# Optimization experiments

Measured on AMD Instinct MI355X. Metric: run time of the kernel, lower is better.

The kernel has to match this reference:

```python
import jax, jax.numpy as jnp
import numpy as np

N_NODES = 100000
N_EDGES = 1600000
IN_CH = 512
HID_CH = 256
OUT_CH = 32
K = 10


def setup_inputs() -> dict:
    key = jax.random.key(0)
    k_x, k_e, k_w1, k_b1, k_w2, k_b2 = jax.random.split(key, 6)
    x = jax.random.normal(k_x, (N_NODES, IN_CH), dtype=jnp.float32)
    edge_index = jax.random.randint(k_e, (2, N_EDGES), 0, N_NODES, dtype=jnp.int64)
    s1 = 1.0 / np.sqrt(IN_CH)
    s2 = 1.0 / np.sqrt(HID_CH)
    W1 = jax.random.uniform(k_w1, (IN_CH, HID_CH), jnp.float32, -s1, s1)
    b1 = jax.random.uniform(k_b1, (HID_CH,), jnp.float32, -s1, s1)
    W2 = jax.random.uniform(k_w2, (HID_CH, OUT_CH), jnp.float32, -s2, s2)
    b2 = jax.random.uniform(k_b2, (OUT_CH,), jnp.float32, -s2, s2)
    gamma = jnp.ones((K + 1,), jnp.float32) / (K + 1)
    return {"x": x, "edge_index": edge_index, "W1": W1, "b1": b1,
            "W2": W2, "b2": b2, "gamma": gamma}


def reference(x, edge_index, W1, b1, W2, b2, gamma):
    # MLP (dropout is identity in eval mode)
    h = jax.nn.relu(x @ W1 + b1) @ W2 + b2  # [N, out]
    row, col = edge_index[0], edge_index[1]
    # symmetric normalization: deg over destination nodes (col)
    deg = jax.ops.segment_sum(jnp.ones((N_EDGES,), h.dtype), col,
                              num_segments=N_NODES)
    deg_inv_sqrt = jnp.where(deg > 0, jax.lax.rsqrt(jnp.maximum(deg, 1.0)), 0.0)
    norm = (deg_inv_sqrt[row] * deg_inv_sqrt[col])[:, None]  # [E, 1]
    out = gamma[0] * h
    h_k = h
    for k in range(1, K + 1):
        # one hop: gather source feats, scale, scatter-add to destinations
        h_k = jax.ops.segment_sum(norm * h_k[row], col, num_segments=N_NODES)
        out = out + gamma[k] * h_k
    return out
```

## Files before the change

### kernel.cpp

```cpp
#include <hip/hip_runtime.h>
#include <hip/hip_bf16.h>

#define NN    100000
#define NE    1600000
#define INCH  512
#define HIDCH 256
#define OUTCH 32
#define KHOPS 10
#define NEPAD (NE + 3 * NN)

typedef __attribute__((ext_vector_type(8))) short short8;
typedef __attribute__((ext_vector_type(4))) float f32x4;

#define GLOAD_LDS16(gsrc, ldst) \
  __builtin_amdgcn_global_load_lds((const __attribute__((address_space(1))) void*)(gsrc), \
                                   (__attribute__((address_space(3))) void*)(ldst), 16, 0, 0)

constexpr size_t ws_align(size_t x) { return (x + 255) & ~(size_t)255; }
constexpr size_t USZ = ws_align((size_t)(NN + 1) * 16 * 2);
constexpr size_t OSZ = ws_align((size_t)NN * 16 * 4);
constexpr size_t OFF_H1   = 0;
constexpr size_t OFF_U00  = OFF_H1   + ws_align((size_t)NN*HIDCH*2);
constexpr size_t OFF_U01  = OFF_U00  + USZ;
constexpr size_t OFF_U10  = OFF_U01  + USZ;
constexpr size_t OFF_U11  = OFF_U10  + USZ;
constexpr size_t OFF_OA0  = OFF_U11  + USZ;
constexpr size_t OFF_OA1  = OFF_OA0  + OSZ;
constexpr size_t OFF_W1TH = OFF_OA1  + OSZ;
constexpr size_t OFF_W1TL = OFF_W1TH + ws_align((size_t)HIDCH*INCH*2);
constexpr size_t OFF_W2TH = OFF_W1TL + ws_align((size_t)HIDCH*INCH*2);
constexpr size_t OFF_W2TL = OFF_W2TH + ws_align((size_t)OUTCH*HIDCH*2);
constexpr size_t OFF_DEG  = OFF_W2TL + ws_align((size_t)OUTCH*HIDCH*2);
constexpr size_t OFF_DIS  = OFF_DEG  + ws_align((size_t)NN*4);
constexpr size_t OFF_RP   = OFF_DIS  + ws_align((size_t)NN*4);
constexpr size_t OFF_CUR  = OFF_RP   + ws_align((size_t)(NN+1)*4);
constexpr size_t OFF_CSR  = OFF_CUR  + ws_align((size_t)NN*4);
constexpr size_t OFF_PART = OFF_CSR  + ws_align((size_t)NEPAD*4);
constexpr size_t OFF_OFFS = OFF_PART + ws_align(512);

__device__ __forceinline__ unsigned short bf16_rne(float f) {
  unsigned int u = __float_as_uint(f);
  u += 0x7fffu + ((u >> 16) & 1u);
  return (unsigned short)(u >> 16);
}
__device__ __forceinline__ float bf16_to_f32(unsigned short h) {
  return __uint_as_float(((unsigned int)h) << 16);
}
__device__ __forceinline__ float bflo(unsigned int w) {
  return __uint_as_float(w << 16);
}
__device__ __forceinline__ float bfhi(unsigned int w) {
  return __uint_as_float(w & 0xffff0000u);
}

__global__ __launch_bounds__(256) void k_count_deg(const int* __restrict__ col,
                                                   int* __restrict__ deg) {
  int e = blockIdx.x * 256 + threadIdx.x;
  if (e < NE) atomicAdd(&deg[col[e]], 1);
}

__global__ __launch_bounds__(256) void k_dis(const int* __restrict__ deg,
                                             float* __restrict__ dis,
                                             unsigned short* u00, unsigned short* u01,
                                             unsigned short* u10, unsigned short* u11) {
  int v = blockIdx.x * 256 + threadIdx.x;
  if (v < NN) {
    int d = deg[v];
    dis[v] = d > 0 ? rsqrtf((float)d) : 0.0f;
  }
  if (blockIdx.x == 0) {
    int t = threadIdx.x;
    if (t < 8)       ((unsigned int*)u00)[(size_t)NN * 8 + t] = 0;
    else if (t < 16) ((unsigned int*)u01)[(size_t)NN * 8 + (t - 8)] = 0;
    else if (t < 24) ((unsigned int*)u10)[(size_t)NN * 8 + (t - 16)] = 0;
    else if (t < 32) ((unsigned int*)u11)[(size_t)NN * 8 + (t - 24)] = 0;
  }
}

__global__ __launch_bounds__(256) void k_scan1(const int* __restrict__ deg,
                                               int* __restrict__ rp,
                                               int* __restrict__ part) {
  __shared__ int s[256];
  int b = blockIdx.x, t = threadIdx.x;
  int base = b * 1024 + t * 4;
  int v0 = (base + 0 < NN) ? ((deg[base + 0] + 3) & ~3) : 0;
  int v1 = (base + 1 < NN) ? ((deg[base + 1] + 3) & ~3) : 0;
  int v2 = (base + 2 < NN) ? ((deg[base + 2] + 3) & ~3) : 0;
  int v3 = (base + 3 < NN) ? ((deg[base + 3] + 3) & ~3) : 0;
  int tot = v0 + v1 + v2 + v3;
  s[t] = tot;
  __syncthreads();
  for (int d = 1; d < 256; d <<= 1) {
    int x = (t >= d) ? s[t - d] : 0;
    __syncthreads();
    s[t] += x;
    __syncthreads();
  }
  int excl = s[t] - tot;
  if (t == 255) part[b] = s[255];
  if (base + 0 < NN) rp[base + 0] = excl;
  if (base + 1 < NN) rp[base + 1] = excl + v0;
  if (base + 2 < NN) rp[base + 2] = excl + v0 + v1;
  if (base + 3 < NN) rp[base + 3] = excl + v0 + v1 + v2;
}

__global__ __launch_bounds__(128) void k_scan2(const int* __restrict__ part,
                                               int* __restrict__ offs) {
  __shared__ int s[128];
  int t = threadIdx.x;
  int v = (t < 98) ? part[t] : 0;
  s[t] = v;
  __syncthreads();
  for (int d = 1; d < 128; d <<= 1) {
    int x = (t >= d) ? s[t - d] : 0;
    __syncthreads();
    s[t] += x;
    __syncthreads();
  }
  if (t < 98) offs[t] = s[t] - v;
}

__global__ __launch_bounds__(256) void k_scan3(int* __restrict__ rp,
                                               const int* __restrict__ offs,
                                               const int* __restrict__ part,
                                               int* __restrict__ cur) {
  int b = blockIdx.x, t = threadIdx.x;
  int o = offs[b];
  int base = b * 1024 + t * 4;
#pragma unroll
  for (int j = 0; j < 4; ++j) {
    int i = base + j;
    if (i < NN) {
      int r = rp[i] + o;
      rp[i] = r;
      cur[i] = r;
    }
  }
  if (b == 0 && t == 0) rp[NN] = offs[97] + part[97];
}

__global__ __launch_bounds__(256) void k_fill(const int* __restrict__ ei,
                                              int* __restrict__ cur,
                                              int* __restrict__ csrc) {
  int e = blockIdx.x * 256 + threadIdx.x;
  if (e < NE) {
    int c = ei[NE + e];
    int p = atomicAdd(&cur[c], 1);
    csrc[p] = ei[e];
  }
}

__global__ __launch_bounds__(256) void k_pad(const int* __restrict__ cur,
                                             const int* __restrict__ rp,
                                             int* __restrict__ csrc) {
  int v = blockIdx.x * 256 + threadIdx.x;
  if (v < NN) {
    int p = cur[v], e = rp[v + 1];
    for (; p < e; ++p) csrc[p] = NN;
  }
}

__global__ __launch_bounds__(256) void k_splitT(const float* __restrict__ src,
                                                unsigned short* __restrict__ dh,
                                                unsigned short* __restrict__ dl,
                                                int K, int N) {
  int idx = blockIdx.x * 256 + threadIdx.x;
  if (idx >= K * N) return;
  int n = idx / K, k = idx - n * K;
  float v = src[(size_t)k * N + n];
  unsigned short h = bf16_rne(v);
  dh[idx] = h;
  dl[idx] = bf16_rne(v - bf16_to_f32(h));
}

__global__ __launch_bounds__(512, 2) void k_gemm1(const float* __restrict__ X,
                                                  const unsigned short* __restrict__ W1Th,
                                                  const unsigned short* __restrict__ W1Tl,
                                                  const float* __restrict__ bias1,
                                                  unsigned short* __restrict__ H1bf) {
  __shared__ __align__(16) unsigned short Ah[2][4096];
  __shared__ __align__(16) unsigned short Bh[2][8192], Bl[2][8192];
  const int t = threadIdx.x;
  const int m0 = blockIdx.x * 128;
  const int w = t >> 6, lane = t & 63;
  const int wm = w >> 2, wn = w & 3;

  const int arow = t >> 2;
  const int achk = t & 3;
  int axrow = m0 + arow; if (axrow >= NN) axrow = NN - 1;
  const float* aptr = X + (size_t)axrow * INCH + achk * 8;
  int aidx = (arow >> 4) * 512 + ((arow & 15) + achk * 16) * 8;
  aidx ^= ((aidx >> 7) & 3) << 4;
  const int aroff = (lane * 8) ^ (((lane >> 4) & 3) << 4);

  const int bn0 = (w * 16) + (lane & 15);
  const int bko = (lane >> 4) * 8;
  const unsigned short* bs0 = W1Th + (size_t)bn0 * INCH + bko;
  const unsigned short* bs1 = W1Th + (size_t)(bn0 + 128) * INCH + bko;
  const unsigned short* bs2 = W1Tl + (size_t)bn0 * INCH + bko;
  const unsigned short* bs3 = W1Tl + (size_t)(bn0 + 128) * INCH + bko;

  f32x4 acc[4][4] = {};
  float4 av0, av1;

  av0 = *(const float4*)(aptr);
  av1 = *(const float4*)(aptr + 4);
  GLOAD_LDS16(bs0, &Bh[0][w * 512]);
  GLOAD_LDS16(bs1, &Bh[0][(w + 8) * 512]);
  GLOAD_LDS16(bs2, &Bl[0][w * 512]);
  GLOAD_LDS16(bs3, &Bl[0][(w + 8) * 512]);
  {
    float af[8] = {av0.x, av0.y, av0.z, av0.w, av1.x, av1.y, av1.z, av1.w};
    short8 ah;
#pragma unroll
    for (int i = 0; i < 8; ++i) {
      unsigned int u = __float_as_uint(af[i]);
      ah[i] = (short)((u + 0x7fffu + ((u >> 16) & 1u)) >> 16);
    }
    *(short8*)&Ah[0][aidx] = ah;
  }
  __syncthreads();

#pragma unroll
  for (int it = 0; it < 16; ++it) {
    const int cur = it & 1, nxt = cur ^ 1;
    const int k0 = it * 32;
    if (it < 15) {
      av0 = *(const float4*)(aptr + k0 + 32);
      av1 = *(const float4*)(aptr + k0 + 36);
      GLOAD_LDS16(bs0 + k0 + 32, &Bh[nxt][w * 512]);
      GLOAD_LDS16(bs1 + k0 + 32, &Bh[nxt][(w + 8) * 512]);
      GLOAD_LDS16(bs2 + k0 + 32, &Bl[nxt][w * 512]);
      GLOAD_LDS16(bs3 + k0 + 32, &Bl[nxt][(w + 8) * 512]);
    }
    short8 afrag[4];
#pragma unroll
    for (int mf = 0; mf < 4; ++mf)
      afrag[mf] = *(const short8*)&Ah[cur][(wm * 4 + mf) * 512 + aroff];
#pragma unroll
    for (int nf = 0; nf < 4; ++nf) {
      short8 bfh = *(const short8*)&Bh[cur][(wn * 4 + nf) * 512 + lane * 8];
      short8 bfl = *(const short8*)&Bl[cur][(wn * 4 + nf) * 512 + lane * 8];
#pragma unroll
      for (int mf = 0; mf < 4; ++mf) {
        acc[mf][nf] = __builtin_amdgcn_mfma_f32_16x16x32_bf16(afrag[mf], bfh, acc[mf][nf], 0, 0, 0);
        acc[mf][nf] = __builtin_amdgcn_mfma_f32_16x16x32_bf16(afrag[mf], bfl, acc[mf][nf], 0, 0, 0);
      }
    }
    if (it < 15) {
      float af[8] = {av0.x, av0.y, av0.z, av0.w, av1.x, av1.y, av1.z, av1.w};
      short8 ah;
#pragma unroll
      for (int i = 0; i < 8; ++i) {
        unsigned int u = __float_as_uint(af[i]);
        ah[i] = (short)((u + 0x7fffu + ((u >> 16) & 1u)) >> 16);
      }
      *(short8*)&Ah[nxt][aidx] = ah;
    }
    __syncthreads();
  }

  const int colbase = wn * 64 + (lane & 15);
  const int rowbase = m0 + wm * 64 + ((lane >> 4) << 2);
#pragma unroll
  for (int nf = 0; nf < 4; ++nf) {
    int col = colbase + nf * 16;
    float b = bias1[col];
#pragma unroll
    for (int mf = 0; mf < 4; ++mf) {
#pragma unroll
      for (int r = 0; r < 4; ++r) {
        int row = rowbase + mf * 16 + r;
        if (row < NN) {
          float h = fmaxf(acc[mf][nf][r] + b, 0.f);
          H1bf[(size_t)row * HIDCH + col] = bf16_rne(h);
        }
      }
    }
  }
}

__global__ __launch_bounds__(256) void k_gemm2(const unsigned short* __restrict__ H1bf,
                                               const unsigned short* __restrict__ W2Th,
                                               const unsigned short* __restrict__ W2Tl,
                                               const float* __restrict__ bias2,
                                               const float* __restrict__ gamma,
                                               const float* __restrict__ dis,
                                               unsigned short* __restrict__ u00,
                                               unsigned short* __restrict__ u01,
                                               float* __restrict__ oa0,
                                               float* __restrict__ oa1) {
  __shared__ __align__(16) unsigned short A2[8192];
  __shared__ __align__(16) unsigned short B2h[2048], B2l[2048];
  const int t = threadIdx.x;
  const int m0 = blockIdx.x * 128;

  const int arow = t >> 1;
  int axrow = m0 + arow; if (axrow >= NN) axrow = NN - 1;
  const int akb = (t & 1) * 32;
  const unsigned short* ap = H1bf + (size_t)axrow * HIDCH + akb;
  const int abase = ((arow >> 4) * 2 + (akb >> 5)) * 512 + (arow & 15) * 8;

  const int bnr = t >> 3, bkq = (t & 7) * 8;
  const int bslot = ((bnr >> 4) * 2 + (bkq >> 5)) * 512 +
                    ((bnr & 15) + (((bkq & 31) >> 3) << 4)) * 8;
  const unsigned short* bhp = W2Th + (size_t)bnr * HIDCH + bkq;
  const unsigned short* blp = W2Tl + (size_t)bnr * HIDCH + bkq;

  const int w = t >> 6, lane = t & 63;

  f32x4 acc[2][2] = {};

  for (int k0 = 0; k0 < HIDCH; k0 += 64) {
    uint4 a0 = *(const uint4*)(ap + k0);
    uint4 a1 = *(const uint4*)(ap + k0 + 8);
    uint4 a2 = *(const uint4*)(ap + k0 + 16);
    uint4 a3 = *(const uint4*)(ap + k0 + 24);
    uint4 bh = *(const uint4*)(bhp + k0);
    uint4 bl = *(const uint4*)(blp + k0);

    __syncthreads();

    *(uint4*)&A2[abase + 0 * 128] = a0;
    *(uint4*)&A2[abase + 1 * 128] = a1;
    *(uint4*)&A2[abase + 2 * 128] = a2;
    *(uint4*)&A2[abase + 3 * 128] = a3;
    *(uint4*)&B2h[bslot] = bh;
    *(uint4*)&B2l[bslot] = bl;

    __syncthreads();

    const short8* AV  = (const short8*)A2;
    const short8* BHV = (const short8*)B2h;
    const short8* BLV = (const short8*)B2l;
#pragma unroll
    for (int k32 = 0; k32 < 2; ++k32) {
      short8 bfh[2], bfl[2];
#pragma unroll
      for (int nf = 0; nf < 2; ++nf) {
        bfh[nf] = BHV[(nf * 2 + k32) * 64 + lane];
        bfl[nf] = BLV[(nf * 2 + k32) * 64 + lane];
      }
#pragma unroll
      for (int mf = 0; mf < 2; ++mf) {
        short8 a = AV[((w * 2 + mf) * 2 + k32) * 64 + lane];
#pragma unroll
        for (int nf = 0; nf < 2; ++nf) {
          acc[mf][nf] = __builtin_amdgcn_mfma_f32_16x16x32_bf16(a, bfh[nf], acc[mf][nf], 0, 0, 0);
          acc[mf][nf] = __builtin_amdgcn_mfma_f32_16x16x32_bf16(a, bfl[nf], acc[mf][nf], 0, 0, 0);
        }
      }
    }
  }

  const float g0 = gamma[0];
  const int colb = lane & 15;
  const int rowb = m0 + w * 32 + ((lane >> 4) << 2);
  const float b2c0 = bias2[colb], b2c1 = bias2[16 + colb];
#pragma unroll
  for (int mf = 0; mf < 2; ++mf) {
#pragma unroll
    for (int r = 0; r < 4; ++r) {
      int row = rowb + mf * 16 + r;
      if (row < NN) {
        float dv = dis[row];
        float h0 = acc[mf][0][r] + b2c0;
        float h1 = acc[mf][1][r] + b2c1;
        size_t o = (size_t)row * 16 + colb;
        u00[o] = bf16_rne(dv * h0);
        u01[o] = bf16_rne(dv * h1);
        oa0[o] = g0 * h0;
        oa1[o] = g0 * h1;
      }
    }
  }
}

__global__ __launch_bounds__(256) void k_hop(
    const unsigned short* __restrict__ uin0, const unsigned short* __restrict__ uin1,
    unsigned short* __restrict__ uout0, unsigned short* __restrict__ uout1,
    float* __restrict__ oa0, float* __restrict__ oa1,
    const int* __restrict__ rp, const int* __restrict__ csrc,
    const float* __restrict__ dis, const float* __restrict__ gamma, int k) {
  const int bid = blockIdx.x;
  const int xcd = bid & 7;
  const int half = xcd >> 2;
  const int hidx = (bid >> 3) * 4 + (xcd & 3);
  if (hidx >= NN / 32) return;
  const unsigned short* __restrict__ Uin = half ? uin1 : uin0;
  unsigned short* __restrict__ Uout = half ? uout1 : uout0;
  float* __restrict__ oacc = half ? oa1 : oa0;

  const int t = threadIdx.x;
  const int g = t >> 3;
  const int li = t & 7;
  const int v = hidx * 32 + g;
  const int s = rp[v], e = rp[v + 1];

  float ax0 = 0.f, ay0 = 0.f, ax1 = 0.f, ay1 = 0.f;
  float ax2 = 0.f, ay2 = 0.f, ax3 = 0.f, ay3 = 0.f;
  int j = s;
  for (; j + 8 <= e; j += 8) {
    int4 sa = *(const int4*)&csrc[j];
    int4 sb = *(const int4*)&csrc[j + 4];
    unsigned int w0 = *(const unsigned int*)&Uin[(size_t)sa.x * 16 + li * 2];
    unsigned int w1 = *(const unsigned int*)&Uin[(size_t)sa.y * 16 + li * 2];
    unsigned int w2 = *(const unsigned int*)&Uin[(size_t)sa.z * 16 + li * 2];
    unsigned int w3 = *(const unsigned int*)&Uin[(size_t)sa.w * 16 + li * 2];
    unsigned int w4 = *(const unsigned int*)&Uin[(size_t)sb.x * 16 + li * 2];
    unsigned int w5 = *(const unsigned int*)&Uin[(size_t)sb.y * 16 + li * 2];
    unsigned int w6 = *(const unsigned int*)&Uin[(size_t)sb.z * 16 + li * 2];
    unsigned int w7 = *(const unsigned int*)&Uin[(size_t)sb.w * 16 + li * 2];
    ax0 += bflo(w0); ay0 += bfhi(w0);
    ax1 += bflo(w1); ay1 += bfhi(w1);
    ax2 += bflo(w2); ay2 += bfhi(w2);
    ax3 += bflo(w3); ay3 += bfhi(w3);
    ax0 += bflo(w4); ay0 += bfhi(w4);
    ax1 += bflo(w5); ay1 += bfhi(w5);
    ax2 += bflo(w6); ay2 += bfhi(w6);
    ax3 += bflo(w7); ay3 += bfhi(w7);
  }
  if (j < e) {
    int4 sa = *(const int4*)&csrc[j];
    unsigned int w0 = *(const unsigned int*)&Uin[(size_t)sa.x * 16 + li * 2];
    unsigned int w1 = *(const unsigned int*)&Uin[(size_t)sa.y * 16 + li * 2];
    unsigned int w2 = *(const unsigned int*)&Uin[(size_t)sa.z * 16 + li * 2];
    unsigned int w3 = *(const unsigned int*)&Uin[(size_t)sa.w * 16 + li * 2];
    ax0 += bflo(w0); ay0 += bfhi(w0);
    ax1 += bflo(w1); ay1 += bfhi(w1);
    ax2 += bflo(w2); ay2 += bfhi(w2);
    ax3 += bflo(w3); ay3 += bfhi(w3);
  }
  const float Sx = (ax0 + ax1) + (ax2 + ax3);
  const float Sy = (ay0 + ay1) + (ay2 + ay3);
  const float dv = dis[v];
  const float gd = gamma[k] * dv;
  const float d2 = dv * dv;
  unsigned int packed = (unsigned int)bf16_rne(d2 * Sx) |
                        ((unsigned int)bf16_rne(d2 * Sy) << 16);
  ((unsigned int*)Uout)[(size_t)v * 8 + li] = packed;
  float2 po = *(const float2*)&oacc[(size_t)v * 16 + li * 2];
  po.x = fmaf(gd, Sx, po.x);
  po.y = fmaf(gd, Sy, po.y);
  *(float2*)&oacc[(size_t)v * 16 + li * 2] = po;
}

__global__ __launch_bounds__(256) void k_merge(const float* __restrict__ oa0,
                                               const float* __restrict__ oa1,
                                               float* __restrict__ out) {
  int i4 = blockIdx.x * 256 + threadIdx.x;
  if (i4 >= NN * 8) return;
  int v = i4 >> 3;
  int j = (i4 & 7) * 4;
  const float* src = (j < 16) ? oa0 : oa1;
  float4 val = *(const float4*)&src[(size_t)v * 16 + (j & 15)];
  *(float4*)&out[(size_t)v * 32 + j] = val;
}

extern "C" void kernel_launch(void* const* d_in, const int* in_sizes, int n_in,
                              void* d_out, int out_size, void* d_ws, size_t ws_size,
                              hipStream_t stream) {
  const float* x     = (const float*)d_in[0];
  const int*   ei    = (const int*)d_in[1];
  const float* W1    = (const float*)d_in[2];
  const float* b1    = (const float*)d_in[3];
  const float* W2    = (const float*)d_in[4];
  const float* b2    = (const float*)d_in[5];
  const float* gamma = (const float*)d_in[6];
  float* out = (float*)d_out;

  char* ws = (char*)d_ws;
  unsigned short* h1bf = (unsigned short*)(ws + OFF_H1);
  unsigned short* U[2][2] = {
    {(unsigned short*)(ws + OFF_U00), (unsigned short*)(ws + OFF_U01)},
    {(unsigned short*)(ws + OFF_U10), (unsigned short*)(ws + OFF_U11)}};
  float* oa0 = (float*)(ws + OFF_OA0);
  float* oa1 = (float*)(ws + OFF_OA1);
  unsigned short* w1th = (unsigned short*)(ws + OFF_W1TH);
  unsigned short* w1tl = (unsigned short*)(ws + OFF_W1TL);
  unsigned short* w2th = (unsigned short*)(ws + OFF_W2TH);
  unsigned short* w2tl = (unsigned short*)(ws + OFF_W2TL);
  int*   deg  = (int*)(ws + OFF_DEG);
  float* dis  = (float*)(ws + OFF_DIS);
  int*   rp   = (int*)(ws + OFF_RP);
  int*   cur  = (int*)(ws + OFF_CUR);
  int*   csrc = (int*)(ws + OFF_CSR);
  int*   part = (int*)(ws + OFF_PART);
  int*   offs = (int*)(ws + OFF_OFFS);

  hipMemsetAsync(deg, 0, NN * sizeof(int), stream);

  k_splitT<<<(INCH * HIDCH + 255) / 256, 256, 0, stream>>>(W1, w1th, w1tl, INCH, HIDCH);
  k_splitT<<<(HIDCH * OUTCH + 255) / 256, 256, 0, stream>>>(W2, w2th, w2tl, HIDCH, OUTCH);

  k_count_deg<<<(NE + 255) / 256, 256, 0, stream>>>(ei + NE, deg);
  k_dis<<<(NN + 255) / 256, 256, 0, stream>>>(deg, dis, U[0][0], U[0][1], U[1][0], U[1][1]);
  k_scan1<<<98, 256, 0, stream>>>(deg, rp, part);
  k_scan2<<<1, 128, 0, stream>>>(part, offs);
  k_scan3<<<98, 256, 0, stream>>>(rp, offs, part, cur);
  k_fill<<<(NE + 255) / 256, 256, 0, stream>>>(ei, cur, csrc);
  k_pad<<<(NN + 255) / 256, 256, 0, stream>>>(cur, rp, csrc);

  k_gemm1<<<(NN + 127) / 128, 512, 0, stream>>>(x, w1th, w1tl, b1, h1bf);
  k_gemm2<<<(NN + 127) / 128, 256, 0, stream>>>(h1bf, w2th, w2tl, b2, gamma, dis,
                                                U[0][0], U[0][1], oa0, oa1);

  const int hop_grid = ((NN / 32 + 3) / 4) * 8;
  for (int k = 1; k <= KHOPS; ++k) {
    const int pin = (k - 1) & 1, pout = k & 1;
    k_hop<<<hop_grid, 256, 0, stream>>>(U[pin][0], U[pin][1], U[pout][0], U[pout][1],
                                        oa0, oa1, rp, csrc, dis, gamma, k);
  }

  k_merge<<<(NN * 8 + 255) / 256, 256, 0, stream>>>(oa0, oa1, out);
}
```

Before: 606.9 us.

## Merge split feature halves into one 32-wide layout and retile GEMM1

The propagation state is no longer split into two 16-channel halves routed to separate XCD groups. It now uses a single 32-channel bf16 buffer, and the hop kernel accumulates directly into the output, so the final merge kernel is removed. GEMM1 changes from a 512-thread, double-buffered, LDS-swizzled 128x256 tile to a 256-thread, single-buffered 128x128 tile on a 2D grid. This gives more blocks but drops the prefetch overlap and the LDS swizzle, and it reads each row of X twice. The hop gather now fetches 64-byte rows per source, which changes cache locality against the earlier per-XCD split.

```diff
diff --git a/kernel.cpp b/kernel.cpp
--- a/kernel.cpp
+++ b/kernel.cpp
@@ -17,16 +17,11 @@
                                    (__attribute__((address_space(3))) void*)(ldst), 16, 0, 0)
 
 constexpr size_t ws_align(size_t x) { return (x + 255) & ~(size_t)255; }
-constexpr size_t USZ = ws_align((size_t)(NN + 1) * 16 * 2);
-constexpr size_t OSZ = ws_align((size_t)NN * 16 * 4);
+constexpr size_t USZ = ws_align((size_t)(NN + 1) * 32 * 2);
 constexpr size_t OFF_H1   = 0;
-constexpr size_t OFF_U00  = OFF_H1   + ws_align((size_t)NN*HIDCH*2);
-constexpr size_t OFF_U01  = OFF_U00  + USZ;
-constexpr size_t OFF_U10  = OFF_U01  + USZ;
-constexpr size_t OFF_U11  = OFF_U10  + USZ;
-constexpr size_t OFF_OA0  = OFF_U11  + USZ;
-constexpr size_t OFF_OA1  = OFF_OA0  + OSZ;
-constexpr size_t OFF_W1TH = OFF_OA1  + OSZ;
+constexpr size_t OFF_U0   = OFF_H1   + ws_align((size_t)NN*HIDCH*2);
+constexpr size_t OFF_U1   = OFF_U0   + USZ;
+constexpr size_t OFF_W1TH = OFF_U1   + USZ;
 constexpr size_t OFF_W1TL = OFF_W1TH + ws_align((size_t)HIDCH*INCH*2);
 constexpr size_t OFF_W2TH = OFF_W1TL + ws_align((size_t)HIDCH*INCH*2);
 constexpr size_t OFF_W2TL = OFF_W2TH + ws_align((size_t)OUTCH*HIDCH*2);
@@ -61,8 +56,7 @@
 
 __global__ __launch_bounds__(256) void k_dis(const int* __restrict__ deg,
                                              float* __restrict__ dis,
-                                             unsigned short* u00, unsigned short* u01,
-                                             unsigned short* u10, unsigned short* u11) {
+                                             unsigned short* u0, unsigned short* u1) {
   int v = blockIdx.x * 256 + threadIdx.x;
   if (v < NN) {
     int d = deg[v];
@@ -70,10 +64,8 @@
   }
   if (blockIdx.x == 0) {
     int t = threadIdx.x;
-    if (t < 8)       ((unsigned int*)u00)[(size_t)NN * 8 + t] = 0;
-    else if (t < 16) ((unsigned int*)u01)[(size_t)NN * 8 + (t - 8)] = 0;
-    else if (t < 24) ((unsigned int*)u10)[(size_t)NN * 8 + (t - 16)] = 0;
-    else if (t < 32) ((unsigned int*)u11)[(size_t)NN * 8 + (t - 24)] = 0;
+    if (t < 16)      ((unsigned int*)u0)[(size_t)NN * 16 + t] = 0;
+    else if (t < 32) ((unsigned int*)u1)[(size_t)NN * 16 + (t - 16)] = 0;
   }
 }
 
@@ -173,94 +165,76 @@
   dl[idx] = bf16_rne(v - bf16_to_f32(h));
 }
 
-__global__ __launch_bounds__(512, 2) void k_gemm1(const float* __restrict__ X,
-                                                  const unsigned short* __restrict__ W1Th,
-                                                  const unsigned short* __restrict__ W1Tl,
-                                                  const float* __restrict__ bias1,
-                                                  unsigned short* __restrict__ H1bf) {
-  __shared__ __align__(16) unsigned short Ah[2][4096];
-  __shared__ __align__(16) unsigned short Bh[2][8192], Bl[2][8192];
+__global__ __launch_bounds__(256) void k_gemm1(const float* __restrict__ X,
+                                               const unsigned short* __restrict__ W1Th,
+                                               const unsigned short* __restrict__ W1Tl,
+                                               const float* __restrict__ bias1,
+                                               unsigned short* __restrict__ H1bf) {
+  __shared__ __align__(16) unsigned short Ah[4096], Bh[4096], Bl[4096];
   const int t = threadIdx.x;
   const int m0 = blockIdx.x * 128;
+  const int n0 = blockIdx.y * 128;
   const int w = t >> 6, lane = t & 63;
-  const int wm = w >> 2, wn = w & 3;
-
-  const int arow = t >> 2;
-  const int achk = t & 3;
+  const int wm = w >> 1, wn = w & 1;
+
+  const int arow = t >> 1;
   int axrow = m0 + arow; if (axrow >= NN) axrow = NN - 1;
-  const float* aptr = X + (size_t)axrow * INCH + achk * 8;
-  int aidx = (arow >> 4) * 512 + ((arow & 15) + achk * 16) * 8;
-  aidx ^= ((aidx >> 7) & 3) << 4;
-  const int aroff = (lane * 8) ^ (((lane >> 4) & 3) << 4);
-
-  const int bn0 = (w * 16) + (lane & 15);
+  const float* aptr = X + (size_t)axrow * INCH + (t & 1) * 16;
+  const int aidx0 = (arow >> 4) * 512 + ((arow & 15) + (t & 1) * 32) * 8;
+  const int aidx1 = aidx0 + 128;
+
   const int bko = (lane >> 4) * 8;
-  const unsigned short* bs0 = W1Th + (size_t)bn0 * INCH + bko;
-  const unsigned short* bs1 = W1Th + (size_t)(bn0 + 128) * INCH + bko;
-  const unsigned short* bs2 = W1Tl + (size_t)bn0 * INCH + bko;
-  const unsigned short* bs3 = W1Tl + (size_t)(bn0 + 128) * INCH + bko;
+  const unsigned short* bs0 = W1Th + (size_t)(n0 + w * 16 + (lane & 15)) * INCH + bko;
+  const unsigned short* bs1 = W1Th + (size_t)(n0 + (w + 4) * 16 + (lane & 15)) * INCH + bko;
+  const unsigned short* bs2 = W1Tl + (size_t)(n0 + w * 16 + (lane & 15)) * INCH + bko;
+  const unsigned short* bs3 = W1Tl + (size_t)(n0 + (w + 4) * 16 + (lane & 15)) * INCH + bko;
 
   f32x4 acc[4][4] = {};
-  float4 av0, av1;
-
-  av0 = *(const float4*)(aptr);
-  av1 = *(const float4*)(aptr + 4);
-  GLOAD_LDS16(bs0, &Bh[0][w * 512]);
-  GLOAD_LDS16(bs1, &Bh[0][(w + 8) * 512]);
-  GLOAD_LDS16(bs2, &Bl[0][w * 512]);
-  GLOAD_LDS16(bs3, &Bl[0][(w + 8) * 512]);
-  {
-    float af[8] = {av0.x, av0.y, av0.z, av0.w, av1.x, av1.y, av1.z, av1.w};
-    short8 ah;
-#pragma unroll
-    for (int i = 0; i < 8; ++i) {
-      unsigned int u = __float_as_uint(af[i]);
-      ah[i] = (short)((u + 0x7fffu + ((u >> 16) & 1u)) >> 16);
-    }
-    *(short8*)&Ah[0][aidx] = ah;
-  }
-  __syncthreads();
-
-#pragma unroll
+
+#pragma unroll 4
   for (int it = 0; it < 16; ++it) {
-    const int cur = it & 1, nxt = cur ^ 1;
     const int k0 = it * 32;
-    if (it < 15) {
-      av0 = *(const float4*)(aptr + k0 + 32);
-      av1 = *(const float4*)(aptr + k0 + 36);
-      GLOAD_LDS16(bs0 + k0 + 32, &Bh[nxt][w * 512]);
-      GLOAD_LDS16(bs1 + k0 + 32, &Bh[nxt][(w + 8) * 512]);
-      GLOAD_LDS16(bs2 + k0 + 32, &Bl[nxt][w * 512]);
-      GLOAD_LDS16(bs3 + k0 + 32, &Bl[nxt][(w + 8) * 512]);
-    }
+    __syncthreads();
+    GLOAD_LDS16(bs0 + k0, &Bh[w * 512]);
+    GLOAD_LDS16(bs1 + k0, &Bh[(w + 4) * 512]);
+    GLOAD_LDS16(bs2 + k0, &Bl[w * 512]);
+    GLOAD_LDS16(bs3 + k0, &Bl[(w + 4) * 512]);
+    {
+      float4 x0 = *(const float4*)(aptr + k0);
+      float4 x1 = *(const float4*)(aptr + k0 + 4);
+      float4 x2 = *(const float4*)(aptr + k0 + 8);
+      float4 x3 = *(const float4*)(aptr + k0 + 12);
+      float af[16] = {x0.x, x0.y, x0.z, x0.w, x1.x, x1.y, x1.z, x1.w,
+                      x2.x, x2.y, x2.z, x2.w, x3.x, x3.y, x3.z, x3.w};
+      short8 a0, a1;
+#pragma unroll
+      for (int i = 0; i < 8; ++i) {
+        unsigned int u = __float_as_uint(af[i]);
+        a0[i] = (short)((u + 0x7fffu + ((u >> 16) & 1u)) >> 16);
+        unsigned int u2 = __float_as_uint(af[8 + i]);
+        a1[i] = (short)((u2 + 0x7fffu + ((u2 >> 16) & 1u)) >> 16);
+      }
+      *(short8*)&Ah[aidx0] = a0;
+      *(short8*)&Ah[aidx1] = a1;
+    }
+    __syncthreads();
     short8 afrag[4];
 #pragma unroll
     for (int mf = 0; mf < 4; ++mf)
-      afrag[mf] = *(const short8*)&Ah[cur][(wm * 4 + mf) * 512 + aroff];
+      afrag[mf] = *(const short8*)&Ah[(wm * 4 + mf) * 512 + lane * 8];
 #pragma unroll
     for (int nf = 0; nf < 4; ++nf) {
-      short8 bfh = *(const short8*)&Bh[cur][(wn * 4 + nf) * 512 + lane * 8];
-      short8 bfl = *(const short8*)&Bl[cur][(wn * 4 + nf) * 512 + lane * 8];
+      short8 bfh = *(const short8*)&Bh[(wn * 4 + nf) * 512 + lane * 8];
+      short8 bfl = *(const short8*)&Bl[(wn * 4 + nf) * 512 + lane * 8];
 #pragma unroll
       for (int mf = 0; mf < 4; ++mf) {
         acc[mf][nf] = __builtin_amdgcn_mfma_f32_16x16x32_bf16(afrag[mf], bfh, acc[mf][nf], 0, 0, 0);
         acc[mf][nf] = __builtin_amdgcn_mfma_f32_16x16x32_bf16(afrag[mf], bfl, acc[mf][nf], 0, 0, 0);
       }
     }
-    if (it < 15) {
-      float af[8] = {av0.x, av0.y, av0.z, av0.w, av1.x, av1.y, av1.z, av1.w};
-      short8 ah;
-#pragma unroll
-      for (int i = 0; i < 8; ++i) {
-        unsigned int u = __float_as_uint(af[i]);
-        ah[i] = (short)((u + 0x7fffu + ((u >> 16) & 1u)) >> 16);
-      }
-      *(short8*)&Ah[nxt][aidx] = ah;
-    }
-    __syncthreads();
-  }
-
-  const int colbase = wn * 64 + (lane & 15);
+  }
+
+  const int colbase = n0 + wn * 64 + (lane & 15);
   const int rowbase = m0 + wm * 64 + ((lane >> 4) << 2);
 #pragma unroll
   for (int nf = 0; nf < 4; ++nf) {
@@ -286,10 +260,8 @@
                                                const float* __restrict__ bias2,
                                                const float* __restrict__ gamma,
                                                const float* __restrict__ dis,
-                                               unsigned short* __restrict__ u00,
-                                               unsigned short* __restrict__ u01,
-                                               float* __restrict__ oa0,
-                                               float* __restrict__ oa1) {
+                                               unsigned short* __restrict__ u0,
+                                               float* __restrict__ out) {
   __shared__ __align__(16) unsigned short A2[8192];
   __shared__ __align__(16) unsigned short B2h[2048], B2l[2048];
   const int t = threadIdx.x;
@@ -366,36 +338,30 @@
         float dv = dis[row];
         float h0 = acc[mf][0][r] + b2c0;
         float h1 = acc[mf][1][r] + b2c1;
-        size_t o = (size_t)row * 16 + colb;
-        u00[o] = bf16_rne(dv * h0);
-        u01[o] = bf16_rne(dv * h1);
-        oa0[o] = g0 * h0;
-        oa1[o] = g0 * h1;
-      }
-    }
-  }
-}
-
-__global__ __launch_bounds__(256) void k_hop(
-    const unsigned short* __restrict__ uin0, const unsigned short* __restrict__ uin1,
-    unsigned short* __restrict__ uout0, unsigned short* __restrict__ uout1,
-    float* __restrict__ oa0, float* __restrict__ oa1,
-    const int* __restrict__ rp, const int* __restrict__ csrc,
-    const float* __restrict__ dis, const float* __restrict__ gamma, int k) {
-  const int bid = blockIdx.x;
-  const int xcd = bid & 7;
-  const int half = xcd >> 2;
-  const int hidx = (bid >> 3) * 4 + (xcd & 3);
-  if (hidx >= NN / 32) return;
-  const unsigned short* __restrict__ Uin = half ? uin1 : uin0;
-  unsigned short* __restrict__ Uout = half ? uout1 : uout0;
-  float* __restrict__ oacc = half ? oa1 : oa0;
-
+        size_t o = (size_t)row * 32 + colb;
+        u0[o] = bf16_rne(dv * h0);
+        u0[o + 16] = bf16_rne(dv * h1);
+        out[o] = g0 * h0;
+        out[o + 16] = g0 * h1;
+      }
+    }
+  }
+}
+
+__global__ __launch_bounds__(256) void k_hop(const unsigned short* __restrict__ Uin,
+                                             unsigned short* __restrict__ Uout,
+                                             float* __restrict__ out,
+                                             const int* __restrict__ rp,
+                                             const int* __restrict__ csrc,
+                                             const float* __restrict__ dis,
+                                             const float* __restrict__ gamma,
+                                             int k) {
   const int t = threadIdx.x;
-  const int g = t >> 3;
-  const int li = t & 7;
-  const int v = hidx * 32 + g;
+  const int g = t >> 4;
+  const int li = t & 15;
+  const int v = blockIdx.x * 16 + g;
   const int s = rp[v], e = rp[v + 1];
+  const unsigned int* Uin32 = (const unsigned int*)Uin;
 
   float ax0 = 0.f, ay0 = 0.f, ax1 = 0.f, ay1 = 0.f;
   float ax2 = 0.f, ay2 = 0.f, ax3 = 0.f, ay3 = 0.f;
@@ -403,14 +369,14 @@
   for (; j + 8 <= e; j += 8) {
     int4 sa = *(const int4*)&csrc[j];
     int4 sb = *(const int4*)&csrc[j + 4];
-    unsigned int w0 = *(const unsigned int*)&Uin[(size_t)sa.x * 16 + li * 2];
-    unsigned int w1 = *(const unsigned int*)&Uin[(size_t)sa.y * 16 + li * 2];
-    unsigned int w2 = *(const unsigned int*)&Uin[(size_t)sa.z * 16 + li * 2];
-    unsigned int w3 = *(const unsigned int*)&Uin[(size_t)sa.w * 16 + li * 2];
-    unsigned int w4 = *(const unsigned int*)&Uin[(size_t)sb.x * 16 + li * 2];
-    unsigned int w5 = *(const unsigned int*)&Uin[(size_t)sb.y * 16 + li * 2];
-    unsigned int w6 = *(const unsigned int*)&Uin[(size_t)sb.z * 16 + li * 2];
-    unsigned int w7 = *(const unsigned int*)&Uin[(size_t)sb.w * 16 + li * 2];
+    unsigned int w0 = Uin32[(size_t)sa.x * 16 + li];
+    unsigned int w1 = Uin32[(size_t)sa.y * 16 + li];
+    unsigned int w2 = Uin32[(size_t)sa.z * 16 + li];
+    unsigned int w3 = Uin32[(size_t)sa.w * 16 + li];
+    unsigned int w4 = Uin32[(size_t)sb.x * 16 + li];
+    unsigned int w5 = Uin32[(size_t)sb.y * 16 + li];
+    unsigned int w6 = Uin32[(size_t)sb.z * 16 + li];
+    unsigned int w7 = Uin32[(size_t)sb.w * 16 + li];
     ax0 += bflo(w0); ay0 += bfhi(w0);
     ax1 += bflo(w1); ay1 += bfhi(w1);
     ax2 += bflo(w2); ay2 += bfhi(w2);
@@ -422,10 +388,10 @@
   }
   if (j < e) {
     int4 sa = *(const int4*)&csrc[j];
-    unsigned int w0 = *(const unsigned int*)&Uin[(size_t)sa.x * 16 + li * 2];
-    unsigned int w1 = *(const unsigned int*)&Uin[(size_t)sa.y * 16 + li * 2];
-    unsigned int w2 = *(const unsigned int*)&Uin[(size_t)sa.z * 16 + li * 2];
-    unsigned int w3 = *(const unsigned int*)&Uin[(size_t)sa.w * 16 + li * 2];
+    unsigned int w0 = Uin32[(size_t)sa.x * 16 + li];
+    unsigned int w1 = Uin32[(size_t)sa.y * 16 + li];
+    unsigned int w2 = Uin32[(size_t)sa.z * 16 + li];
+    unsigned int w3 = Uin32[(size_t)sa.w * 16 + li];
     ax0 += bflo(w0); ay0 += bfhi(w0);
     ax1 += bflo(w1); ay1 += bfhi(w1);
     ax2 += bflo(w2); ay2 += bfhi(w2);
@@ -438,23 +404,12 @@
   const float d2 = dv * dv;
   unsigned int packed = (unsigned int)bf16_rne(d2 * Sx) |
                         ((unsigned int)bf16_rne(d2 * Sy) << 16);
-  ((unsigned int*)Uout)[(size_t)v * 8 + li] = packed;
-  float2 po = *(const float2*)&oacc[(size_t)v * 16 + li * 2];
+  ((unsigned int*)Uout)[(size_t)v * 16 + li] = packed;
+  const size_t o = (size_t)v * 32 + li * 2;
+  float2 po = *(const float2*)&out[o];
   po.x = fmaf(gd, Sx, po.x);
   po.y = fmaf(gd, Sy, po.y);
-  *(float2*)&oacc[(size_t)v * 16 + li * 2] = po;
-}
-
-__global__ __launch_bounds__(256) void k_merge(const float* __restrict__ oa0,
-                                               const float* __restrict__ oa1,
-                                               float* __restrict__ out) {
-  int i4 = blockIdx.x * 256 + threadIdx.x;
-  if (i4 >= NN * 8) return;
-  int v = i4 >> 3;
-  int j = (i4 & 7) * 4;
-  const float* src = (j < 16) ? oa0 : oa1;
-  float4 val = *(const float4*)&src[(size_t)v * 16 + (j & 15)];
-  *(float4*)&out[(size_t)v * 32 + j] = val;
+  *(float2*)&out[o] = po;
 }
 
 extern "C" void kernel_launch(void* const* d_in, const int* in_sizes, int n_in,
@@ -471,11 +426,8 @@
 
   char* ws = (char*)d_ws;
   unsigned short* h1bf = (unsigned short*)(ws + OFF_H1);
-  unsigned short* U[2][2] = {
-    {(unsigned short*)(ws + OFF_U00), (unsigned short*)(ws + OFF_U01)},
-    {(unsigned short*)(ws + OFF_U10), (unsigned short*)(ws + OFF_U11)}};
-  float* oa0 = (float*)(ws + OFF_OA0);
-  float* oa1 = (float*)(ws + OFF_OA1);
+  unsigned short* U[2] = {(unsigned short*)(ws + OFF_U0),
+                          (unsigned short*)(ws + OFF_U1)};
   unsigned short* w1th = (unsigned short*)(ws + OFF_W1TH);
   unsigned short* w1tl = (unsigned short*)(ws + OFF_W1TL);
   unsigned short* w2th = (unsigned short*)(ws + OFF_W2TH);
@@ -494,23 +446,19 @@
   k_splitT<<<(HIDCH * OUTCH + 255) / 256, 256, 0, stream>>>(W2, w2th, w2tl, HIDCH, OUTCH);
 
   k_count_deg<<<(NE + 255) / 256, 256, 0, stream>>>(ei + NE, deg);
-  k_dis<<<(NN + 255) / 256, 256, 0, stream>>>(deg, dis, U[0][0], U[0][1], U[1][0], U[1][1]);
+  k_dis<<<(NN + 255) / 256, 256, 0, stream>>>(deg, dis, U[0], U[1]);
   k_scan1<<<98, 256, 0, stream>>>(deg, rp, part);
   k_scan2<<<1, 128, 0, stream>>>(part, offs);
   k_scan3<<<98, 256, 0, stream>>>(rp, offs, part, cur);
   k_fill<<<(NE + 255) / 256, 256, 0, stream>>>(ei, cur, csrc);
   k_pad<<<(NN + 255) / 256, 256, 0, stream>>>(cur, rp, csrc);
 
-  k_gemm1<<<(NN + 127) / 128, 512, 0, stream>>>(x, w1th, w1tl, b1, h1bf);
+  k_gemm1<<<dim3((NN + 127) / 128, 2), 256, 0, stream>>>(x, w1th, w1tl, b1, h1bf);
   k_gemm2<<<(NN + 127) / 128, 256, 0, stream>>>(h1bf, w2th, w2tl, b2, gamma, dis,
-                                                U[0][0], U[0][1], oa0, oa1);
-
-  const int hop_grid = ((NN / 32 + 3) / 4) * 8;
+                                                U[0], out);
+
   for (int k = 1; k <= KHOPS; ++k) {
-    const int pin = (k - 1) & 1, pout = k & 1;
-    k_hop<<<hop_grid, 256, 0, stream>>>(U[pin][0], U[pin][1], U[pout][0], U[pout][1],
-                                        oa0, oa1, rp, csrc, dis, gamma, k);
-  }
-
-  k_merge<<<(NN * 8 + 255) / 256, 256, 0, stream>>>(oa0, oa1, out);
-}
+    k_hop<<<NN / 16, 256, 0, stream>>>(U[(k - 1) & 1], U[k & 1], out,
+                                       rp, csrc, dis, gamma, k);
+  }
+}
```

After: 608.0 us. About the same (+0.2%).
